# Kernel tuning notes

Hardware: AMD Instinct MI355X
Metric: run time of the kernel (lower is better)

The kernel has to match this reference:

```python
import jax, jax.numpy as jnp
import numpy as np

DIN = 1024
DIM = 1024
NUM_HEADS = 16
HEAD_DIM = DIM // NUM_HEADS
SEQ_LEN = 2048
BATCH = 2


def setup_inputs() -> dict:
    key = jax.random.key(0)
    ks = jax.random.split(key, 5)
    s = 0.02
    x = jax.random.normal(ks[0], (BATCH, SEQ_LEN, DIN), dtype=jnp.float32)
    # torch nn.Linear weights are (out_features, in_features)
    wq = jax.random.normal(ks[1], (DIM, DIN), dtype=jnp.float32) * s
    wk = jax.random.normal(ks[2], (DIM, DIN), dtype=jnp.float32) * s
    wv = jax.random.normal(ks[3], (DIM, DIN), dtype=jnp.float32) * s
    wo = jax.random.normal(ks[4], (DIM, DIM), dtype=jnp.float32) * s
    return {"x": x, "wq": wq, "wk": wk, "wv": wv, "wo": wo}


def reference(x, wq, wk, wv, wo):
    bs, seq_len, _ = x.shape
    # project and split heads: [b, h, s, d]
    def split(z):
        return z.reshape(bs, seq_len, NUM_HEADS, HEAD_DIM).transpose(0, 2, 1, 3)
    q = split(x @ wq.T)
    k = split(x @ wk.T)
    v = split(x @ wv.T)
    # raw scores, causal mask applied BEFORE the 1/sqrt(d) scaling (as in source;
    # -inf is invariant to positive scaling so math matches standard causal attn)
    att = jnp.einsum('bhqd,bhkd->bhqk', q, k)
    causal = jnp.triu(jnp.ones((seq_len, seq_len), dtype=bool), k=1)
    att = jnp.where(causal, -jnp.inf, att)
    att = jax.nn.softmax(att / jnp.sqrt(jnp.float32(HEAD_DIM)), axis=-1)
    ctx = jnp.einsum('bhqk,bhkd->bhqd', att, v)
    ctx = ctx.transpose(0, 2, 1, 3).reshape(bs, seq_len, DIM)
    return ctx @ wo.T
```

## Files before the change

### kernel.cpp

```cpp
#include <hip/hip_runtime.h>
#include <stdint.h>

#define DIN 1024
#define DIMM 1024
#define NH 16
#define HD 64
#define SEQ 2048
#define BATCH 2
#define MTOT (BATCH*SEQ)
#define SCALE 0.125f

typedef __bf16 bf16;
typedef __bf16 bf16x8 __attribute__((ext_vector_type(8)));
typedef __bf16 bf16x4 __attribute__((ext_vector_type(4)));
typedef float f32x4 __attribute__((ext_vector_type(4)));

__device__ __forceinline__ void async16(bf16* lds, const bf16* g) {
  __builtin_amdgcn_global_load_lds(
      (const __attribute__((address_space(1))) void*)g,
      (__attribute__((address_space(3))) void*)lds, 16, 0, 0);
}

#define WAIT_VM(n)  asm volatile("s_waitcnt vmcnt(" #n ")" ::: "memory")
#define BARRIER()   asm volatile("s_barrier" ::: "memory")

__global__ __launch_bounds__(256) void convert_all(const float* __restrict__ x,
                                                   const float* __restrict__ wq,
                                                   const float* __restrict__ wk,
                                                   const float* __restrict__ wv,
                                                   const float* __restrict__ wo,
                                                   bf16* __restrict__ xb,
                                                   bf16* __restrict__ Wb) {
  const int t = blockIdx.x * 256 + threadIdx.x;
#pragma unroll
  for (int i = 0; i < 4; ++i) {
    const int c = t + i * 262144;
    const float* src;
    bf16* dst;
    if (c < 524288) {
      src = x + (size_t)c * 8;
      dst = xb + (size_t)c * 8;
    } else {
      const int cw = c - 524288;
      const int w = cw >> 17;
      const int off = (cw & 131071) * 8;
      const float* wp = (w == 0) ? wq : (w == 1) ? wk : (w == 2) ? wv : wo;
      src = wp + off;
      dst = Wb + (size_t)w * 1048576 + off;
    }
    f32x4 a = *(const f32x4*)src;
    f32x4 b = *(const f32x4*)(src + 4);
    bf16x8 r;
    r[0] = (bf16)a[0]; r[1] = (bf16)a[1]; r[2] = (bf16)a[2]; r[3] = (bf16)a[3];
    r[4] = (bf16)b[0]; r[5] = (bf16)b[1]; r[6] = (bf16)b[2]; r[7] = (bf16)b[3];
    *(bf16x8*)dst = r;
  }
}

__global__ __launch_bounds__(256, 2) void qkv_gemm(const bf16* __restrict__ A,
                                                   const bf16* __restrict__ B,
                                                   bf16* __restrict__ Q,
                                                   bf16* __restrict__ Kb,
                                                   bf16* __restrict__ Vt) {
  __shared__ bf16 As0[128 * 64];
  __shared__ bf16 As1[128 * 64];
  __shared__ bf16 Bs0[192 * 64];
  __shared__ bf16 Bs1[192 * 64];
  const int tid  = threadIdx.x;
  const int lane = tid & 63;
  const int wave = tid >> 6;
  const int lrow = lane & 15;
  const int quad = lane >> 4;
  const int wrow = wave >> 1;
  const int wcol = wave & 1;
  const int lin  = blockIdx.x;
  const int xcd  = lin & 7;
  const int idx  = lin >> 3;
  const int nbase = (xcd * 2 + (idx & 1)) * 192;
  const int mbase = (idx >> 1) * 128;

  const int srow = tid >> 3;
  const int sdst = srow * 64 + (tid & 7) * 8;
  const int sx   = ((tid & 7) ^ (srow & 7)) * 8;

  const bf16* ap = A + (size_t)(mbase + srow) * DIN + sx;
  const bf16* bp = B + (size_t)(nbase + srow) * DIN + sx;

  f32x4 acc[4][6] = {};

#define QKV_STAGE(Asb, Bsb)                                          \
  do {                                                               \
    _Pragma("unroll")                                                \
    for (int i = 0; i < 4; ++i)                                      \
      async16(&Asb[sdst + i * 2048], ap + (size_t)i * 32 * DIN);     \
    _Pragma("unroll")                                                \
    for (int i = 0; i < 6; ++i)                                      \
      async16(&Bsb[sdst + i * 2048], bp + (size_t)i * 32 * DIN);     \
  } while (0)

#define QKV_COMPUTE(Asb, Bsb)                                        \
  do {                                                               \
    __builtin_amdgcn_s_setprio(1);                                   \
    _Pragma("unroll")                                                \
    for (int h = 0; h < 2; ++h) {                                    \
      const int cx = ((h * 4 + quad) ^ (lrow & 7)) * 8;              \
      bf16x8 af[4], bfr[6];                                          \
      _Pragma("unroll")                                              \
      for (int i = 0; i < 4; ++i)                                    \
        af[i] = *(const bf16x8*)&Asb[(wrow * 64 + i * 16 + lrow) * 64 + cx]; \
      _Pragma("unroll")                                              \
      for (int j = 0; j < 6; ++j)                                    \
        bfr[j] = *(const bf16x8*)&Bsb[(wcol * 96 + j * 16 + lrow) * 64 + cx]; \
      _Pragma("unroll")                                              \
      for (int i = 0; i < 4; ++i)                                    \
        _Pragma("unroll")                                            \
        for (int j = 0; j < 6; ++j)                                  \
          acc[i][j] = __builtin_amdgcn_mfma_f32_16x16x32_bf16(af[i], bfr[j], acc[i][j], 0, 0, 0); \
    }                                                                \
    __builtin_amdgcn_s_setprio(0);                                   \
  } while (0)

  QKV_STAGE(As0, Bs0);
  WAIT_VM(0);
  BARRIER();

#pragma unroll 1
  for (int t = 0; t < 16; t += 2) {
    ap += 64; bp += 64;
    QKV_STAGE(As1, Bs1);
    WAIT_VM(10);
    BARRIER();
    QKV_COMPUTE(As0, Bs0);
    BARRIER();
    if (t + 2 < 16) {
      ap += 64; bp += 64;
      QKV_STAGE(As0, Bs0);
      WAIT_VM(10);
    } else {
      WAIT_VM(0);
    }
    BARRIER();
    QKV_COMPUTE(As1, Bs1);
    BARRIER();
  }

#undef QKV_STAGE
#undef QKV_COMPUTE

  const float C1 = 0.18033688f;
#pragma unroll
  for (int mt = 0; mt < 4; ++mt) {
    const int m0 = mbase + wrow * 64 + mt * 16 + quad * 4;
#pragma unroll
    for (int nt = 0; nt < 6; ++nt) {
      const int n16 = nbase + wcol * 96 + nt * 16;
      const int n = n16 + lrow;
      if (n16 < 1024) {
#pragma unroll
        for (int rr = 0; rr < 4; ++rr)
          Q[(size_t)(m0 + rr) * 1024 + n] = (bf16)(acc[mt][nt][rr] * C1);
      } else if (n16 < 2048) {
#pragma unroll
        for (int rr = 0; rr < 4; ++rr)
          Kb[(size_t)(m0 + rr) * 1024 + (n - 1024)] = (bf16)acc[mt][nt][rr];
      } else {
        const int nn = n - 2048;
        const int row = ((m0 >> 11) * 16 + (nn >> 6)) * 64 + (nn & 63);
        bf16x4 ov;
#pragma unroll
        for (int rr = 0; rr < 4; ++rr) ov[rr] = (bf16)acc[mt][nt][rr];
        *(bf16x4*)&Vt[(size_t)row * SEQ + (m0 & 2047)] = ov;
      }
    }
  }
}

__global__ __launch_bounds__(256, 2) void proj_gemm(const bf16* __restrict__ A,
                                                    const bf16* __restrict__ B,
                                                    float* __restrict__ C) {
  __shared__ bf16 As0[128 * 64];
  __shared__ bf16 As1[128 * 64];
  __shared__ bf16 Bs0[64 * 64];
  __shared__ bf16 Bs1[64 * 64];
  const int tid  = threadIdx.x;
  const int lane = tid & 63;
  const int wave = tid >> 6;
  const int lrow = lane & 15;
  const int quad = lane >> 4;
  const int wr = (wave >> 1) * 64;
  const int wc = (wave & 1) * 32;
  const int lin = blockIdx.x;
  const int xcd = lin & 7;
  const int idx = lin >> 3;
  const int nbase = (xcd * 2 + (idx & 1)) * 64;
  const int mbase = (idx >> 1) * 128;
  const int srow = tid >> 3;
  const int sdst = srow * 64 + (tid & 7) * 8;
  const int sx   = ((tid & 7) ^ (srow & 7)) * 8;

  const bf16* ap = A + (size_t)(mbase + srow) * DIMM + sx;
  const bf16* bp = B + (size_t)(nbase + srow) * DIMM + sx;

  f32x4 acc[4][2] = {};

#define PRJ_STAGE(Asb, Bsb)                                          \
  do {                                                               \
    _Pragma("unroll")                                                \
    for (int i = 0; i < 4; ++i)                                      \
      async16(&Asb[sdst + i * 2048], ap + (size_t)i * 32 * DIMM);    \
    _Pragma("unroll")                                                \
    for (int i = 0; i < 2; ++i)                                      \
      async16(&Bsb[sdst + i * 2048], bp + (size_t)i * 32 * DIMM);    \
  } while (0)

#define PRJ_COMPUTE(Asb, Bsb)                                        \
  do {                                                               \
    __builtin_amdgcn_s_setprio(1);                                   \
    _Pragma("unroll")                                                \
    for (int h = 0; h < 2; ++h) {                                    \
      const int cx = ((h * 4 + quad) ^ (lrow & 7)) * 8;              \
      bf16x8 af[4], bfr[2];                                          \
      _Pragma("unroll")                                              \
      for (int i = 0; i < 4; ++i)                                    \
        af[i] = *(const bf16x8*)&Asb[(wr + i * 16 + lrow) * 64 + cx]; \
      _Pragma("unroll")                                              \
      for (int i = 0; i < 2; ++i)                                    \
        bfr[i] = *(const bf16x8*)&Bsb[(wc + i * 16 + lrow) * 64 + cx]; \
      _Pragma("unroll")                                              \
      for (int mt = 0; mt < 4; ++mt)                                 \
        _Pragma("unroll")                                            \
        for (int nt = 0; nt < 2; ++nt)                               \
          acc[mt][nt] = __builtin_amdgcn_mfma_f32_16x16x32_bf16(af[mt], bfr[nt], acc[mt][nt], 0, 0, 0); \
    }                                                                \
    __builtin_amdgcn_s_setprio(0);                                   \
  } while (0)

  PRJ_STAGE(As0, Bs0);
  WAIT_VM(0);
  BARRIER();

#pragma unroll 1
  for (int t = 0; t < 16; t += 2) {
    ap += 64; bp += 64;
    PRJ_STAGE(As1, Bs1);
    WAIT_VM(6);
    BARRIER();
    PRJ_COMPUTE(As0, Bs0);
    BARRIER();
    if (t + 2 < 16) {
      ap += 64; bp += 64;
      PRJ_STAGE(As0, Bs0);
      WAIT_VM(6);
    } else {
      WAIT_VM(0);
    }
    BARRIER();
    PRJ_COMPUTE(As1, Bs1);
    BARRIER();
  }

#undef PRJ_STAGE
#undef PRJ_COMPUTE

#pragma unroll
  for (int mt = 0; mt < 4; ++mt) {
    const int m0 = mbase + wr + mt * 16 + quad * 4;
#pragma unroll
    for (int nt = 0; nt < 2; ++nt) {
      const int n = nbase + wc + nt * 16 + lrow;
#pragma unroll
      for (int rr = 0; rr < 4; ++rr)
        C[(size_t)(m0 + rr) * 1024 + n] = acc[mt][nt][rr];
    }
  }
}

__global__ __launch_bounds__(256, 5) void attn(const bf16* __restrict__ Q,
                                               const bf16* __restrict__ K,
                                               const bf16* __restrict__ Vt,
                                               bf16* __restrict__ O) {
  __shared__ bf16 Ks[2][64 * 64];
  __shared__ bf16 Vts[2][64 * 64];
  const int tid  = threadIdx.x;
  const int wave = tid >> 6;
  const int lane = tid & 63;
  const int lrow = lane & 15;
  const int quad = lane >> 4;
  const int lin  = blockIdx.x;
  const int bh   = lin & 31;
  const int pp   = lin >> 5;
  const int b = bh >> 4;
  const int h = bh & 15;

  const bf16* Qh  = Q  + (size_t)(b * SEQ) * DIMM + h * HD;
  const bf16* Kh  = K  + (size_t)(b * SEQ) * DIMM + h * HD;
  const bf16* Vth = Vt + (size_t)bh * 64 * SEQ;

  const int srow = tid >> 3;
  const int sdst = srow * 64 + (tid & 7) * 8;
  const int sx   = ((tid & 7) ^ (srow & 7)) * 8;
  const int cx0 = ((0 + quad) ^ (lrow & 7)) * 8;
  const int cx1 = ((4 + quad) ^ (lrow & 7)) * 8;
  const int LL = lrow & 7;
  const int qh = quad >> 1, ql = quad & 1;
  int vc[4];
#pragma unroll
  for (int g = 0; g < 4; ++g)
    vc[g] = ((((2 * g + qh) ^ LL) << 1) | ql) * 4;

#pragma unroll 1
  for (int seg = 0; seg < 2; ++seg) {
    const int qi = seg ? pp : (31 - pp);
    const int qw = qi * 64 + wave * 16;
    const int ntiles = qi + 1;

    bf16x8 qf0 = *(const bf16x8*)&Qh[(size_t)(qw + lrow) * DIMM + quad * 8];
    bf16x8 qf1 = *(const bf16x8*)&Qh[(size_t)(qw + lrow) * DIMM + 32 + quad * 8];

    const bf16* kg0 = Kh + (size_t)srow * DIMM + sx;
    const bf16* kg1 = kg0 + (size_t)32 * DIMM;
    const bf16* vg0 = Vth + (size_t)srow * SEQ + sx;
    const bf16* vg1 = vg0 + (size_t)32 * SEQ;

    async16(&Ks[0][sdst],         kg0);
    async16(&Ks[0][sdst + 2048],  kg1);
    async16(&Vts[0][sdst],        vg0);
    async16(&Vts[0][sdst + 2048], vg1);
    __syncthreads();

    f32x4 lacc = {};
    f32x4 o_acc[4] = {};
    int cur = 0;

    for (int kt = 0; kt < ntiles; ++kt) {
      if (kt + 1 < ntiles) {
        kg0 += 64 * DIMM; kg1 += 64 * DIMM; vg0 += 64; vg1 += 64;
        bf16* Kn = Ks[cur ^ 1];
        bf16* Vn = Vts[cur ^ 1];
        async16(&Kn[sdst],        kg0);
        async16(&Kn[sdst + 2048], kg1);
        async16(&Vn[sdst],        vg0);
        async16(&Vn[sdst + 2048], vg1);
      }
      const bf16* Kc = Ks[cur];
      const bf16* Vc = Vts[cur];
      f32x4 s[4] = {};
#pragma unroll
      for (int gg = 0; gg < 4; ++gg) {
        bf16x8 kf0 = *(const bf16x8*)&Kc[(gg * 16 + lrow) * 64 + cx0];
        bf16x8 kf1 = *(const bf16x8*)&Kc[(gg * 16 + lrow) * 64 + cx1];
        s[gg] = __builtin_amdgcn_mfma_f32_16x16x32_bf16(kf0, qf0, s[gg], 0, 0, 0);
        s[gg] = __builtin_amdgcn_mfma_f32_16x16x32_bf16(kf1, qf1, s[gg], 0, 0, 0);
      }
      if (kt == qi) {
        const int qrow = qw + lrow;
        const int kbase = kt * 64;
#pragma unroll
        for (int gg = 0; gg < 4; ++gg)
#pragma unroll
          for (int r = 0; r < 4; ++r)
            s[gg][r] = (kbase + gg * 16 + quad * 4 + r > qrow) ? -1e30f : s[gg][r];
      }
      bf16x8 pf0, pf1;
#pragma unroll
      for (int gg = 0; gg < 4; ++gg)
#pragma unroll
        for (int r = 0; r < 4; ++r) {
          const float p = __builtin_amdgcn_exp2f(s[gg][r]);
          lacc[r] += p;
          if (gg < 2) pf0[(gg & 1) * 4 + r] = (bf16)p;
          else        pf1[(gg & 1) * 4 + r] = (bf16)p;
        }
#pragma unroll
      for (int dt = 0; dt < 4; ++dt) {
        const bf16* Vr = &Vc[(dt * 16 + lrow) * 64];
        bf16x4 a0 = *(const bf16x4*)&Vr[vc[0]];
        bf16x4 a1 = *(const bf16x4*)&Vr[vc[1]];
        bf16x4 b0 = *(const bf16x4*)&Vr[vc[2]];
        bf16x4 b1 = *(const bf16x4*)&Vr[vc[3]];
        bf16x8 vfA = __builtin_shufflevector(a0, a1, 0, 1, 2, 3, 4, 5, 6, 7);
        bf16x8 vfB = __builtin_shufflevector(b0, b1, 0, 1, 2, 3, 4, 5, 6, 7);
        o_acc[dt] = __builtin_amdgcn_mfma_f32_16x16x32_bf16(vfA, pf0, o_acc[dt], 0, 0, 0);
        o_acc[dt] = __builtin_amdgcn_mfma_f32_16x16x32_bf16(vfB, pf1, o_acc[dt], 0, 0, 0);
      }
      __syncthreads();
      cur ^= 1;
    }

    float lsum = (lacc[0] + lacc[1]) + (lacc[2] + lacc[3]);
    lsum += __shfl_xor(lsum, 16);
    lsum += __shfl_xor(lsum, 32);
    const float rl = __builtin_amdgcn_rcpf(lsum);
    bf16* Ob = O + (size_t)(b * SEQ + qw + lrow) * DIMM + h * HD;
#pragma unroll
    for (int dt = 0; dt < 4; ++dt) {
      bf16x4 ov;
#pragma unroll
      for (int r = 0; r < 4; ++r)
        ov[r] = (bf16)(o_acc[dt][r] * rl);
      *(bf16x4*)&Ob[dt * 16 + quad * 4] = ov;
    }
  }
}

extern "C" void kernel_launch(void* const* d_in, const int* in_sizes, int n_in,
                              void* d_out, int out_size, void* d_ws, size_t ws_size,
                              hipStream_t stream) {
  const float* x  = (const float*)d_in[0];
  const float* wq = (const float*)d_in[1];
  const float* wk = (const float*)d_in[2];
  const float* wv = (const float*)d_in[3];
  const float* wo = (const float*)d_in[4];

  const size_t M4 = (size_t)MTOT * DIMM;
  bf16* xb  = (bf16*)d_ws;
  bf16* Wb  = xb + M4;
  bf16* Q   = Wb + M4;
  bf16* Kb  = Q + M4;
  bf16* Vt  = Kb + M4;
  bf16* CTX = xb;
  float* out = (float*)d_out;

  convert_all<<<dim3(1024), dim3(256), 0, stream>>>(x, wq, wk, wv, wo, xb, Wb);
  qkv_gemm<<<dim3(512), dim3(256), 0, stream>>>(xb, Wb, Q, Kb, Vt);
  attn<<<dim3(512), dim3(256), 0, stream>>>(Q, Kb, Vt, CTX);
  proj_gemm<<<dim3(512), dim3(256), 0, stream>>>(CTX, Wb + 3 * 1048576, out);
}
```

Baseline: 172.2 us.

## Widen attention key/value tiles to 128 keys per pipeline step

The attention kernel now stages 128 keys and values per iteration instead of 64, which halves the number of loop iterations and barriers and doubles the MFMA work between syncs. LDS buffers double to 64 KB per block, and the launch-bound occupancy hint drops from 5 to 2 blocks. When the diagonal tile lands at an odd index, the last step masks up to 64 extra keys, so some work is wasted. Lower occupancy may reduce latency hiding.

```diff
diff --git a/kernel.cpp b/kernel.cpp
--- a/kernel.cpp
+++ b/kernel.cpp
@@ -275,12 +275,12 @@
   }
 }
 
-__global__ __launch_bounds__(256, 5) void attn(const bf16* __restrict__ Q,
+__global__ __launch_bounds__(256, 2) void attn(const bf16* __restrict__ Q,
                                                const bf16* __restrict__ K,
                                                const bf16* __restrict__ Vt,
                                                bf16* __restrict__ O) {
-  __shared__ bf16 Ks[2][64 * 64];
-  __shared__ bf16 Vts[2][64 * 64];
+  __shared__ bf16 Ks[2][128 * 64];
+  __shared__ bf16 Vts[2][128 * 64];
   const int tid  = threadIdx.x;
   const int wave = tid >> 6;
   const int lane = tid & 63;
@@ -308,80 +308,94 @@
   for (int g = 0; g < 4; ++g)
     vc[g] = ((((2 * g + qh) ^ LL) << 1) | ql) * 4;
 
+#define ATT_STAGE(buf, kg, vg)                                        \
+  do {                                                                \
+    _Pragma("unroll")                                                 \
+    for (int i = 0; i < 4; ++i)                                       \
+      async16(&Ks[buf][sdst + i * 2048], kg + (size_t)i * 32 * DIMM); \
+    async16(&Vts[buf][sdst],        vg);                              \
+    async16(&Vts[buf][sdst + 2048], vg + (size_t)32 * SEQ);           \
+    async16(&Vts[buf][sdst + 4096], vg + 64);                         \
+    async16(&Vts[buf][sdst + 6144], vg + (size_t)32 * SEQ + 64);      \
+  } while (0)
+
 #pragma unroll 1
   for (int seg = 0; seg < 2; ++seg) {
     const int qi = seg ? pp : (31 - pp);
     const int qw = qi * 64 + wave * 16;
-    const int ntiles = qi + 1;
+    const int nt = (qi + 2) >> 1;
 
     bf16x8 qf0 = *(const bf16x8*)&Qh[(size_t)(qw + lrow) * DIMM + quad * 8];
     bf16x8 qf1 = *(const bf16x8*)&Qh[(size_t)(qw + lrow) * DIMM + 32 + quad * 8];
 
-    const bf16* kg0 = Kh + (size_t)srow * DIMM + sx;
-    const bf16* kg1 = kg0 + (size_t)32 * DIMM;
-    const bf16* vg0 = Vth + (size_t)srow * SEQ + sx;
-    const bf16* vg1 = vg0 + (size_t)32 * SEQ;
-
-    async16(&Ks[0][sdst],         kg0);
-    async16(&Ks[0][sdst + 2048],  kg1);
-    async16(&Vts[0][sdst],        vg0);
-    async16(&Vts[0][sdst + 2048], vg1);
+    const bf16* kg = Kh + (size_t)srow * DIMM + sx;
+    const bf16* vg = Vth + (size_t)srow * SEQ + sx;
+
+    ATT_STAGE(0, kg, vg);
     __syncthreads();
 
     f32x4 lacc = {};
     f32x4 o_acc[4] = {};
     int cur = 0;
 
-    for (int kt = 0; kt < ntiles; ++kt) {
-      if (kt + 1 < ntiles) {
-        kg0 += 64 * DIMM; kg1 += 64 * DIMM; vg0 += 64; vg1 += 64;
-        bf16* Kn = Ks[cur ^ 1];
-        bf16* Vn = Vts[cur ^ 1];
-        async16(&Kn[sdst],        kg0);
-        async16(&Kn[sdst + 2048], kg1);
-        async16(&Vn[sdst],        vg0);
-        async16(&Vn[sdst + 2048], vg1);
+    for (int kt = 0; kt < nt; ++kt) {
+      if (kt + 1 < nt) {
+        kg += 128 * DIMM; vg += 128;
+        const int nb = cur ^ 1;
+        ATT_STAGE(nb, kg, vg);
       }
       const bf16* Kc = Ks[cur];
       const bf16* Vc = Vts[cur];
-      f32x4 s[4] = {};
-#pragma unroll
-      for (int gg = 0; gg < 4; ++gg) {
+      f32x4 s[8];
+#pragma unroll
+      for (int gg = 0; gg < 8; ++gg) {
+        s[gg] = f32x4{};
         bf16x8 kf0 = *(const bf16x8*)&Kc[(gg * 16 + lrow) * 64 + cx0];
         bf16x8 kf1 = *(const bf16x8*)&Kc[(gg * 16 + lrow) * 64 + cx1];
         s[gg] = __builtin_amdgcn_mfma_f32_16x16x32_bf16(kf0, qf0, s[gg], 0, 0, 0);
         s[gg] = __builtin_amdgcn_mfma_f32_16x16x32_bf16(kf1, qf1, s[gg], 0, 0, 0);
       }
-      if (kt == qi) {
+      if (kt == nt - 1) {
         const int qrow = qw + lrow;
-        const int kbase = kt * 64;
-#pragma unroll
-        for (int gg = 0; gg < 4; ++gg)
+        const int kbase = kt * 128;
+#pragma unroll
+        for (int gg = 0; gg < 8; ++gg)
 #pragma unroll
           for (int r = 0; r < 4; ++r)
             s[gg][r] = (kbase + gg * 16 + quad * 4 + r > qrow) ? -1e30f : s[gg][r];
       }
-      bf16x8 pf0, pf1;
-#pragma unroll
-      for (int gg = 0; gg < 4; ++gg)
+      bf16x8 pf0, pf1, pf2, pf3;
+#pragma unroll
+      for (int gg = 0; gg < 8; ++gg)
 #pragma unroll
         for (int r = 0; r < 4; ++r) {
           const float p = __builtin_amdgcn_exp2f(s[gg][r]);
           lacc[r] += p;
-          if (gg < 2) pf0[(gg & 1) * 4 + r] = (bf16)p;
-          else        pf1[(gg & 1) * 4 + r] = (bf16)p;
+          if      (gg < 2) pf0[(gg & 1) * 4 + r] = (bf16)p;
+          else if (gg < 4) pf1[(gg & 1) * 4 + r] = (bf16)p;
+          else if (gg < 6) pf2[(gg & 1) * 4 + r] = (bf16)p;
+          else             pf3[(gg & 1) * 4 + r] = (bf16)p;
         }
 #pragma unroll
       for (int dt = 0; dt < 4; ++dt) {
-        const bf16* Vr = &Vc[(dt * 16 + lrow) * 64];
-        bf16x4 a0 = *(const bf16x4*)&Vr[vc[0]];
-        bf16x4 a1 = *(const bf16x4*)&Vr[vc[1]];
-        bf16x4 b0 = *(const bf16x4*)&Vr[vc[2]];
-        bf16x4 b1 = *(const bf16x4*)&Vr[vc[3]];
-        bf16x8 vfA = __builtin_shufflevector(a0, a1, 0, 1, 2, 3, 4, 5, 6, 7);
-        bf16x8 vfB = __builtin_shufflevector(b0, b1, 0, 1, 2, 3, 4, 5, 6, 7);
-        o_acc[dt] = __builtin_amdgcn_mfma_f32_16x16x32_bf16(vfA, pf0, o_acc[dt], 0, 0, 0);
-        o_acc[dt] = __builtin_amdgcn_mfma_f32_16x16x32_bf16(vfB, pf1, o_acc[dt], 0, 0, 0);
+        const bf16* Vr0 = &Vc[(dt * 16 + lrow) * 64];
+        const bf16* Vr1 = &Vc[4096 + (dt * 16 + lrow) * 64];
+        bf16x4 a0 = *(const bf16x4*)&Vr0[vc[0]];
+        bf16x4 a1 = *(const bf16x4*)&Vr0[vc[1]];
+        bf16x4 b0 = *(const bf16x4*)&Vr0[vc[2]];
+        bf16x4 b1 = *(const bf16x4*)&Vr0[vc[3]];
+        bf16x4 c0 = *(const bf16x4*)&Vr1[vc[0]];
+        bf16x4 c1 = *(const bf16x4*)&Vr1[vc[1]];
+        bf16x4 d0 = *(const bf16x4*)&Vr1[vc[2]];
+        bf16x4 d1 = *(const bf16x4*)&Vr1[vc[3]];
+        bf16x8 vA = __builtin_shufflevector(a0, a1, 0, 1, 2, 3, 4, 5, 6, 7);
+        bf16x8 vB = __builtin_shufflevector(b0, b1, 0, 1, 2, 3, 4, 5, 6, 7);
+        bf16x8 vC = __builtin_shufflevector(c0, c1, 0, 1, 2, 3, 4, 5, 6, 7);
+        bf16x8 vD = __builtin_shufflevector(d0, d1, 0, 1, 2, 3, 4, 5, 6, 7);
+        o_acc[dt] = __builtin_amdgcn_mfma_f32_16x16x32_bf16(vA, pf0, o_acc[dt], 0, 0, 0);
+        o_acc[dt] = __builtin_amdgcn_mfma_f32_16x16x32_bf16(vB, pf1, o_acc[dt], 0, 0, 0);
+        o_acc[dt] = __builtin_amdgcn_mfma_f32_16x16x32_bf16(vC, pf2, o_acc[dt], 0, 0, 0);
+        o_acc[dt] = __builtin_amdgcn_mfma_f32_16x16x32_bf16(vD, pf3, o_acc[dt], 0, 0, 0);
       }
       __syncthreads();
       cur ^= 1;
@@ -401,6 +415,7 @@
       *(bf16x4*)&Ob[dt * 16 + quad * 4] = ov;
     }
   }
+#undef ATT_STAGE
 }
 
 extern "C" void kernel_launch(void* const* d_in, const int* in_sizes, int n_in,
```

Result: faster. 162.6 us (-5.6%).
